# Kernel tuning notes

Hardware: AMD Instinct MI355X
Metric: run time of the kernel (lower is better)

## Reference

```python
import jax, jax.numpy as jnp
import numpy as np

EPS = 1e-4

def _mp_normalize(x):
    # EDM2-style normalize: divide by (eps + RMS-scaled L2 norm) along last dim -> unit RMS
    n = jnp.linalg.norm(x, axis=-1, keepdims=True)
    n = EPS + n * (1.0 / np.sqrt(x.shape[-1]))
    return x / n

def _mp_linear(x, w):
    # magnitude-preserving linear: row-normalized weight scaled by 1/sqrt(fan_in), no bias
    fan_in = w.shape[-1]
    w_hat = _mp_normalize(w) * (1.0 / np.sqrt(fan_in))
    return x @ w_hat.T

def setup_inputs() -> dict:
    key = jax.random.key(0)
    k1, k2, k3 = jax.random.split(key, 3)
    B, T, D = 2, 2048, 1024
    x = jax.random.normal(k1, (B, T, D), dtype=jnp.float32)
    w_qkv = jax.random.normal(k2, (3 * D, D), dtype=jnp.float32)
    w_out = jax.random.normal(k3, (D, D), dtype=jnp.float32)
    return {"x": x, "w_qkv": w_qkv, "w_out": w_out}

def reference(x, w_qkv, w_out):
    B, T, D = x.shape
    H = 16
    hd = D // H
    scale = 1.0 / np.sqrt(hd)

    qkv = _mp_linear(x, w_qkv)                      # (B, T, 3D)
    q, k, v = jnp.split(qkv, 3, axis=-1)            # each (B, T, D)

    def to_heads(t):
        return t.reshape(B, T, H, hd).transpose(0, 2, 1, 3)  # (B, H, T, hd)

    q, k, v = to_heads(q), to_heads(k), to_heads(v)
    q = _mp_normalize(q)
    k = _mp_normalize(k)

    scores = jnp.einsum("bhqd,bhkd->bhqk", q, k) * scale
    attn = jax.nn.softmax(scores, axis=-1)
    out = jnp.einsum("bhqk,bhkd->bhqd", attn, v)    # (B, H, T, hd)
    out = out.transpose(0, 2, 1, 3).reshape(B, T, D)
    return _mp_linear(out, w_out)
```

## Files before the change

kernel.cpp:

```cpp
#include <hip/hip_runtime.h>

#define BATCH  2
#define SEQ    2048
#define DMODEL 1024
#define NHEAD  16
#define HDIM   64
#define NROWS  (BATCH * SEQ)
#define QKVC   (3 * DMODEL)

typedef float f32x4 __attribute__((ext_vector_type(4)));
typedef float f32x16 __attribute__((ext_vector_type(16)));
typedef short s16x8 __attribute__((ext_vector_type(8)));
typedef short s16x4 __attribute__((ext_vector_type(4)));
typedef unsigned int u32x4 __attribute__((ext_vector_type(4)));

__device__ __forceinline__ unsigned short f2bf(float f) {
  unsigned int u = __float_as_uint(f);
  u = (u + 0x7FFFu + ((u >> 16) & 1u)) >> 16;
  return (unsigned short)u;
}
__device__ __forceinline__ float bf2f(unsigned short s) {
  return __uint_as_float(((unsigned int)s) << 16);
}
__device__ __forceinline__ unsigned pkbf(float a, float b) {
  unsigned r;
  asm("v_cvt_pk_bf16_f32 %0, %1, %2" : "=v"(r) : "v"(a), "v"(b));
  return r;
}
__device__ __forceinline__ void swp(unsigned &a, unsigned &b) {
  asm volatile("v_permlane32_swap_b32 %0, %1" : "+v"(a), "+v"(b));
}

__global__ __launch_bounds__(256) void k_prep(const float* __restrict__ Wq_src,
                                              const float* __restrict__ Wo_src,
                                              const float* __restrict__ X,
                                              unsigned short* __restrict__ Wq,
                                              unsigned short* __restrict__ Wo,
                                              unsigned short* __restrict__ Xb) {
  const int row = blockIdx.x, tid = threadIdx.x;
  if (row < QKVC + DMODEL) {
    const float* src = (row < QKVC) ? (Wq_src + (size_t)row * DMODEL)
                                    : (Wo_src + (size_t)(row - QKVC) * DMODEL);
    unsigned short* dst = (row < QKVC) ? (Wq + (size_t)row * DMODEL)
                                       : (Wo + (size_t)(row - QKVC) * DMODEL);
    float4 v = ((const float4*)src)[tid];
    float ss = v.x * v.x + v.y * v.y + v.z * v.z + v.w * v.w;
#pragma unroll
    for (int m = 1; m < 64; m <<= 1) ss += __shfl_xor(ss, m);
    __shared__ float part[4];
    if ((tid & 63) == 0) part[tid >> 6] = ss;
    __syncthreads();
    const float tot = part[0] + part[1] + part[2] + part[3];
    const float scale = 0.03125f / (1e-4f + sqrtf(tot) * 0.03125f);
    unsigned short* op = dst + tid * 4;
    op[0] = f2bf(v.x * scale); op[1] = f2bf(v.y * scale);
    op[2] = f2bf(v.z * scale); op[3] = f2bf(v.w * scale);
  } else {
    const int r = row - (QKVC + DMODEL);
    const float4 v = ((const float4*)(X + (size_t)r * DMODEL))[tid];
    ushort4 o = { f2bf(v.x), f2bf(v.y), f2bf(v.z), f2bf(v.w) };
    ((ushort4*)(Xb + (size_t)r * DMODEL))[tid] = o;
  }
}

#define LDP 88
__global__ __launch_bounds__(256, 3) void k_gemm_qkv(const unsigned short* __restrict__ A,
                                                     const unsigned short* __restrict__ Bm,
                                                     unsigned short* __restrict__ C,
                                                     unsigned short* __restrict__ Vt) {
  const int M = NROWS, N = QKVC, K = DMODEL;
  __shared__ unsigned short As[128 * LDP];
  __shared__ unsigned short Bs[128 * LDP];
  const int tid = threadIdx.x;
  const int nbn = N >> 7;
  const int bm = (blockIdx.x / nbn) << 7;
  const int bn = (blockIdx.x % nbn) << 7;
  const int wave = tid >> 6, lane = tid & 63;
  const int wr = (wave >> 1) << 6, wc = (wave & 1) << 6;
  const int l16 = lane & 15, lg = lane >> 4;

  f32x4 acc[4][4];
#pragma unroll
  for (int m = 0; m < 4; ++m)
#pragma unroll
    for (int n = 0; n < 4; ++n) acc[m][n] = (f32x4){0.f, 0.f, 0.f, 0.f};

  s16x8 ra[4], rb[4];
#pragma unroll
  for (int it = 0; it < 4; ++it) {
    const int c = it * 256 + tid;
    const int r = c >> 3, col = (c & 7) << 3;
    ra[it] = *(const s16x8*)(A + (size_t)(bm + r) * K + col);
    rb[it] = *(const s16x8*)(Bm + (size_t)(bn + r) * K + col);
  }

  for (int k0 = 0; k0 < K; k0 += 64) {
    __syncthreads();
#pragma unroll
    for (int it = 0; it < 4; ++it) {
      const int c = it * 256 + tid;
      const int r = c >> 3, col = (c & 7) << 3;
      *(s16x8*)(As + r * LDP + col) = ra[it];
      *(s16x8*)(Bs + r * LDP + col) = rb[it];
    }
    __syncthreads();
    if (k0 + 64 < K) {
#pragma unroll
      for (int it = 0; it < 4; ++it) {
        const int c = it * 256 + tid;
        const int r = c >> 3, col = (c & 7) << 3;
        ra[it] = *(const s16x8*)(A + (size_t)(bm + r) * K + k0 + 64 + col);
        rb[it] = *(const s16x8*)(Bm + (size_t)(bn + r) * K + k0 + 64 + col);
      }
    }
#pragma unroll
    for (int ks = 0; ks < 2; ++ks) {
      s16x8 af[4], bq[4];
#pragma unroll
      for (int m = 0; m < 4; ++m)
        af[m] = *(const s16x8*)(As + (wr + m * 16 + l16) * LDP + ks * 32 + lg * 8);
#pragma unroll
      for (int n = 0; n < 4; ++n)
        bq[n] = *(const s16x8*)(Bs + (wc + n * 16 + l16) * LDP + ks * 32 + lg * 8);
#pragma unroll
      for (int m = 0; m < 4; ++m)
#pragma unroll
        for (int n = 0; n < 4; ++n)
          acc[m][n] = __builtin_amdgcn_mfma_f32_16x16x32_bf16(af[m], bq[n], acc[m][n], 0, 0, 0);
    }
  }

  const int colbase = bn + wc;
  if (colbase < 2 * DMODEL) {
    const float qmul = (colbase < DMODEL) ? 0.125f : 1.0f;
#pragma unroll
    for (int m = 0; m < 4; ++m)
#pragma unroll
      for (int r = 0; r < 4; ++r) {
        float ss = 0.f;
#pragma unroll
        for (int n = 0; n < 4; ++n) ss += acc[m][n][r] * acc[m][n][r];
        ss += __shfl_xor(ss, 1); ss += __shfl_xor(ss, 2);
        ss += __shfl_xor(ss, 4); ss += __shfl_xor(ss, 8);
        const float scale = qmul / (1e-4f + sqrtf(ss) * 0.125f);
#pragma unroll
        for (int n = 0; n < 4; ++n)
          C[(size_t)(bm + wr + m * 16 + lg * 4 + r) * N + (colbase + n * 16 + l16)] =
              f2bf(acc[m][n][r] * scale);
      }
  } else {
    const int hv = (colbase - 2 * DMODEL) >> 6;
    const int token0 = bm + wr;
    const int b_ = token0 >> 11;
    const int bh = b_ * NHEAD + hv;
    const int t0 = (token0 & (SEQ - 1)) + lg * 4;
#pragma unroll
    for (int m = 0; m < 4; ++m)
#pragma unroll
      for (int n = 0; n < 4; ++n) {
        const int d = n * 16 + l16;
        s16x4 ov = { (short)f2bf(acc[m][n][0]), (short)f2bf(acc[m][n][1]),
                     (short)f2bf(acc[m][n][2]), (short)f2bf(acc[m][n][3]) };
        *(s16x4*)(Vt + (size_t)(bh * HDIM + d) * SEQ + t0 + m * 16) = ov;
      }
  }
}

__global__ __launch_bounds__(256, 3) void k_gemm_out(const unsigned short* __restrict__ A,
                                                     const unsigned short* __restrict__ Bm,
                                                     float* __restrict__ C,
                                                     int M, int N, int K) {
  __shared__ unsigned short As[128 * LDP];
  __shared__ unsigned short Bs[128 * LDP];
  const int tid = threadIdx.x;
  const int nbn = N >> 7;
  const int bm = (blockIdx.x / nbn) << 7;
  const int bn = (blockIdx.x % nbn) << 7;
  const int wave = tid >> 6, lane = tid & 63;
  const int wr = (wave >> 1) << 6, wc = (wave & 1) << 6;
  const int l16 = lane & 15, lg = lane >> 4;

  f32x4 acc[4][4];
#pragma unroll
  for (int m = 0; m < 4; ++m)
#pragma unroll
    for (int n = 0; n < 4; ++n) acc[m][n] = (f32x4){0.f, 0.f, 0.f, 0.f};

  s16x8 ra[4], rb[4];
#pragma unroll
  for (int it = 0; it < 4; ++it) {
    const int c = it * 256 + tid;
    const int r = c >> 3, col = (c & 7) << 3;
    ra[it] = *(const s16x8*)(A + (size_t)(bm + r) * K + col);
    rb[it] = *(const s16x8*)(Bm + (size_t)(bn + r) * K + col);
  }

  for (int k0 = 0; k0 < K; k0 += 64) {
    __syncthreads();
#pragma unroll
    for (int it = 0; it < 4; ++it) {
      const int c = it * 256 + tid;
      const int r = c >> 3, col = (c & 7) << 3;
      *(s16x8*)(As + r * LDP + col) = ra[it];
      *(s16x8*)(Bs + r * LDP + col) = rb[it];
    }
    __syncthreads();
    if (k0 + 64 < K) {
#pragma unroll
      for (int it = 0; it < 4; ++it) {
        const int c = it * 256 + tid;
        const int r = c >> 3, col = (c & 7) << 3;
        ra[it] = *(const s16x8*)(A + (size_t)(bm + r) * K + k0 + 64 + col);
        rb[it] = *(const s16x8*)(Bm + (size_t)(bn + r) * K + k0 + 64 + col);
      }
    }
#pragma unroll
    for (int ks = 0; ks < 2; ++ks) {
      s16x8 af[4], bq[4];
#pragma unroll
      for (int m = 0; m < 4; ++m)
        af[m] = *(const s16x8*)(As + (wr + m * 16 + l16) * LDP + ks * 32 + lg * 8);
#pragma unroll
      for (int n = 0; n < 4; ++n)
        bq[n] = *(const s16x8*)(Bs + (wc + n * 16 + l16) * LDP + ks * 32 + lg * 8);
#pragma unroll
      for (int m = 0; m < 4; ++m)
#pragma unroll
        for (int n = 0; n < 4; ++n)
          acc[m][n] = __builtin_amdgcn_mfma_f32_16x16x32_bf16(af[m], bq[n], acc[m][n], 0, 0, 0);
    }
  }
#pragma unroll
  for (int m = 0; m < 4; ++m)
#pragma unroll
    for (int n = 0; n < 4; ++n)
#pragma unroll
      for (int r = 0; r < 4; ++r)
        C[(size_t)(bm + wr + m * 16 + lg * 4 + r) * N + (bn + wc + n * 16 + l16)] =
            acc[m][n][r];
}

__global__ __launch_bounds__(512) void k_attn(const unsigned short* __restrict__ qkv,
                                              const unsigned short* __restrict__ Vt,
                                              unsigned short* __restrict__ O) {
  const int bid = blockIdx.x;
  const int logical = ((bid & 7) << 6) + (bid >> 3);
  const int bh = logical >> 4, qt = logical & 15;
  const int b = bh >> 4, h = bh & 15;
  const int tid = threadIdx.x;
  const int wave = tid >> 6, lane = tid & 63;
  const int l31 = lane & 31, hi = lane >> 5;
  const int qw = wave & 3, half = wave >> 2;
  const int q0 = qt * 128 + qw * 32;

  __shared__ s16x8 smem[2048];
  __shared__ float LL[4][64];

  s16x8* ksh = smem + half * 512;
  s16x8* vsh = smem + 1024 + half * 512;

  const unsigned short* qp =
      qkv + (size_t)(b * SEQ + q0 + l31) * QKVC + h * HDIM + hi * 8;
  const s16x8 qf0 = *(const s16x8*)(qp);
  const s16x8 qf1 = *(const s16x8*)(qp + 16);
  const s16x8 qf2 = *(const s16x8*)(qp + 32);
  const s16x8 qf3 = *(const s16x8*)(qp + 48);

  const int t8 = tid & 255;
  const int srow = t8 >> 3, chunk = t8 & 7;
  const unsigned short* ksrc =
      qkv + (size_t)(b * SEQ + half * 1024 + srow) * QKVC + DMODEL + h * HDIM + chunk * 8;
  const unsigned short* vsrc =
      Vt + (size_t)(bh * HDIM + srow) * SEQ + half * 1024 + chunk * 8;
  const int wsl = srow * 8 + (chunk ^ (srow & 7));
  const int wsh = wsl + 256;

  f32x16 acc0 = {0,0,0,0,0,0,0,0,0,0,0,0,0,0,0,0};
  f32x16 acc1 = {0,0,0,0,0,0,0,0,0,0,0,0,0,0,0,0};
  float l = 0.f;

  for (int kt = 0; kt < 1024; kt += 64) {
    const s16x8 rk0 = *(const s16x8*)(ksrc + (size_t)kt * QKVC);
    const s16x8 rk1 = *(const s16x8*)(ksrc + (size_t)(kt + 32) * QKVC);
    const s16x8 rv0 = *(const s16x8*)(vsrc + kt);
    const s16x8 rv1 = *(const s16x8*)(vsrc + (size_t)32 * SEQ + kt);
    __syncthreads();
    ksh[wsl] = rk0; ksh[wsh] = rk1;
    vsh[wsl] = rv0; vsh[wsh] = rv1;
    __syncthreads();
#pragma unroll
    for (int kh = 0; kh < 2; ++kh) {
      const int key = kh * 32 + l31;
      const int kb = key * 8, kx = key & 7;
      f32x16 st = {0,0,0,0,0,0,0,0,0,0,0,0,0,0,0,0};
      st = __builtin_amdgcn_mfma_f32_32x32x16_bf16(ksh[kb + ((0 + hi) ^ kx)], qf0, st, 0, 0, 0);
      st = __builtin_amdgcn_mfma_f32_32x32x16_bf16(ksh[kb + ((2 + hi) ^ kx)], qf1, st, 0, 0, 0);
      st = __builtin_amdgcn_mfma_f32_32x32x16_bf16(ksh[kb + ((4 + hi) ^ kx)], qf2, st, 0, 0, 0);
      st = __builtin_amdgcn_mfma_f32_32x32x16_bf16(ksh[kb + ((6 + hi) ^ kx)], qf3, st, 0, 0, 0);

#pragma unroll
      for (int r = 0; r < 16; ++r) st[r] = __expf(st[r] - 8.f);

      float s0 = (st[0] + st[1]) + (st[2] + st[3]);
      float s1 = (st[4] + st[5]) + (st[6] + st[7]);
      float s2 = (st[8] + st[9]) + (st[10] + st[11]);
      float s3 = (st[12] + st[13]) + (st[14] + st[15]);
      l += (s0 + s1) + (s2 + s3);

      unsigned P0 = pkbf(st[0], st[1]),   P1 = pkbf(st[2], st[3]);
      unsigned P2 = pkbf(st[4], st[5]),   P3 = pkbf(st[6], st[7]);
      unsigned P4 = pkbf(st[8], st[9]),   P5 = pkbf(st[10], st[11]);
      unsigned P6 = pkbf(st[12], st[13]), P7 = pkbf(st[14], st[15]);
      swp(P0, P2);
      swp(P1, P3);
      swp(P4, P6);
      swp(P5, P7);
      u32x4 w0; w0[0] = P0; w0[1] = P1; w0[2] = P2; w0[3] = P3;
      u32x4 w1; w1[0] = P4; w1[1] = P5; w1[2] = P6; w1[3] = P7;
      const s16x8 pf0 = __builtin_bit_cast(s16x8, w0);
      const s16x8 pf1 = __builtin_bit_cast(s16x8, w1);

      const int vb0 = l31 * 8,        vx0 = l31 & 7;
      const int vb1 = (l31 + 32) * 8, vx1 = vx0;
      acc0 = __builtin_amdgcn_mfma_f32_32x32x16_bf16(vsh[vb0 + ((kh * 4 + 0 + hi) ^ vx0)], pf0, acc0, 0, 0, 0);
      acc0 = __builtin_amdgcn_mfma_f32_32x32x16_bf16(vsh[vb0 + ((kh * 4 + 2 + hi) ^ vx0)], pf1, acc0, 0, 0, 0);
      acc1 = __builtin_amdgcn_mfma_f32_32x32x16_bf16(vsh[vb1 + ((kh * 4 + 0 + hi) ^ vx1)], pf0, acc1, 0, 0, 0);
      acc1 = __builtin_amdgcn_mfma_f32_32x32x16_bf16(vsh[vb1 + ((kh * 4 + 2 + hi) ^ vx1)], pf1, acc1, 0, 0, 0);
    }
  }

  l += __shfl_xor(l, 32);

  __syncthreads();
  float* OO = (float*)smem;
  if (half) {
    float* o_ = OO + qw * 2048;
#pragma unroll
    for (int r = 0; r < 16; ++r) {
      o_[r * 64 + lane] = acc0[r];
      o_[(16 + r) * 64 + lane] = acc1[r];
    }
    LL[qw][lane] = l;
  }
  __syncthreads();
  if (!half) {
    const float inv = 1.f / (l + LL[qw][lane]);
    const float* o_ = OO + qw * 2048;
    unsigned short* ob = O + (size_t)(b * SEQ + q0 + l31) * DMODEL + h * HDIM;
#pragma unroll
    for (int g = 0; g < 4; ++g) {
      float e00 = (acc0[4 * g]     + o_[(4 * g) * 64 + lane])     * inv;
      float e01 = (acc0[4 * g + 1] + o_[(4 * g + 1) * 64 + lane]) * inv;
      float e02 = (acc0[4 * g + 2] + o_[(4 * g + 2) * 64 + lane]) * inv;
      float e03 = (acc0[4 * g + 3] + o_[(4 * g + 3) * 64 + lane]) * inv;
      float e10 = (acc1[4 * g]     + o_[(16 + 4 * g) * 64 + lane])     * inv;
      float e11 = (acc1[4 * g + 1] + o_[(16 + 4 * g + 1) * 64 + lane]) * inv;
      float e12 = (acc1[4 * g + 2] + o_[(16 + 4 * g + 2) * 64 + lane]) * inv;
      float e13 = (acc1[4 * g + 3] + o_[(16 + 4 * g + 3) * 64 + lane]) * inv;
      s16x4 o0 = { (short)f2bf(e00), (short)f2bf(e01), (short)f2bf(e02), (short)f2bf(e03) };
      s16x4 o1 = { (short)f2bf(e10), (short)f2bf(e11), (short)f2bf(e12), (short)f2bf(e13) };
      *(s16x4*)(ob + g * 8 + hi * 4) = o0;
      *(s16x4*)(ob + 32 + g * 8 + hi * 4) = o1;
    }
  }
}

extern "C" void kernel_launch(void* const* d_in, const int* in_sizes, int n_in,
                              void* d_out, int out_size, void* d_ws, size_t ws_size,
                              hipStream_t stream) {
  const float* x    = (const float*)d_in[0];
  const float* wqkv = (const float*)d_in[1];
  const float* wout = (const float*)d_in[2];
  char* ws = (char*)d_ws;
  unsigned short* Wq  = (unsigned short*)(ws);
  unsigned short* Wo  = (unsigned short*)(ws + 6291456);
  unsigned short* Xb  = (unsigned short*)(ws + 8388608);
  unsigned short* QKV = (unsigned short*)(ws + 16777216);
  unsigned short* Vt  = (unsigned short*)(ws + 41943040);
  (void)in_sizes; (void)n_in; (void)out_size; (void)ws_size;

  k_prep<<<QKVC + DMODEL + NROWS, 256, 0, stream>>>(wqkv, wout, x, Wq, Wo, Xb);
  k_gemm_qkv<<<(NROWS / 128) * (QKVC / 128), 256, 0, stream>>>(Xb, Wq, QKV, Vt);
  k_attn<<<BATCH * NHEAD * 16, 512, 0, stream>>>(QKV, Vt, Xb);
  k_gemm_out<<<(NROWS / 128) * (DMODEL / 128), 256, 0, stream>>>(
      Xb, Wo, (float*)d_out, NROWS, DMODEL, DMODEL);
}
```

Measured before the change: 113.6 us.

## Double-buffer K/V shared memory tiles in attention kernel with register prefetch

The attention kernel's K/V staging goes from a single LDS buffer with two barriers per tile to a ping-pong double buffer. Tile it+1 is written from registers while tile it is computed, and global loads for tile it+2 are issued ahead, so each iteration needs only one barrier. This aims to overlap global memory latency with MFMA work and cut synchronisation. In exchange it doubles the LDS footprint to 64KB plus LL and keeps more registers live, which may reduce occupancy.

```diff
diff --git a/kernel.cpp b/kernel.cpp
--- a/kernel.cpp
+++ b/kernel.cpp
@@ -253,11 +253,8 @@
   const int qw = wave & 3, half = wave >> 2;
   const int q0 = qt * 128 + qw * 32;
 
-  __shared__ s16x8 smem[2048];
+  __shared__ s16x8 smem[4096];
   __shared__ float LL[4][64];
-
-  s16x8* ksh = smem + half * 512;
-  s16x8* vsh = smem + 1024 + half * 512;
 
   const unsigned short* qp =
       qkv + (size_t)(b * SEQ + q0 + l31) * QKVC + h * HDIM + hi * 8;
@@ -274,20 +271,42 @@
       Vt + (size_t)(bh * HDIM + srow) * SEQ + half * 1024 + chunk * 8;
   const int wsl = srow * 8 + (chunk ^ (srow & 7));
   const int wsh = wsl + 256;
+  const int koff = half * 512;
+  const int voff = 1024 + half * 512;
 
   f32x16 acc0 = {0,0,0,0,0,0,0,0,0,0,0,0,0,0,0,0};
   f32x16 acc1 = {0,0,0,0,0,0,0,0,0,0,0,0,0,0,0,0};
   float l = 0.f;
 
-  for (int kt = 0; kt < 1024; kt += 64) {
-    const s16x8 rk0 = *(const s16x8*)(ksrc + (size_t)kt * QKVC);
-    const s16x8 rk1 = *(const s16x8*)(ksrc + (size_t)(kt + 32) * QKVC);
-    const s16x8 rv0 = *(const s16x8*)(vsrc + kt);
-    const s16x8 rv1 = *(const s16x8*)(vsrc + (size_t)32 * SEQ + kt);
-    __syncthreads();
-    ksh[wsl] = rk0; ksh[wsh] = rk1;
-    vsh[wsl] = rv0; vsh[wsh] = rv1;
-    __syncthreads();
+  s16x8 rk0 = *(const s16x8*)(ksrc);
+  s16x8 rk1 = *(const s16x8*)(ksrc + (size_t)32 * QKVC);
+  s16x8 rv0 = *(const s16x8*)(vsrc);
+  s16x8 rv1 = *(const s16x8*)(vsrc + (size_t)32 * SEQ);
+  smem[koff + wsl] = rk0; smem[koff + wsh] = rk1;
+  smem[voff + wsl] = rv0; smem[voff + wsh] = rv1;
+  rk0 = *(const s16x8*)(ksrc + (size_t)64 * QKVC);
+  rk1 = *(const s16x8*)(ksrc + (size_t)96 * QKVC);
+  rv0 = *(const s16x8*)(vsrc + 64);
+  rv1 = *(const s16x8*)(vsrc + (size_t)32 * SEQ + 64);
+  __syncthreads();
+
+  int cur = 0;
+  for (int it = 0; it < 16; ++it) {
+    const int base = cur << 11;
+    const int nbase = base ^ 2048;
+    if (it + 1 < 16) {
+      smem[nbase + koff + wsl] = rk0; smem[nbase + koff + wsh] = rk1;
+      smem[nbase + voff + wsl] = rv0; smem[nbase + voff + wsh] = rv1;
+    }
+    if (it + 2 < 16) {
+      const int kt2 = (it + 2) << 6;
+      rk0 = *(const s16x8*)(ksrc + (size_t)kt2 * QKVC);
+      rk1 = *(const s16x8*)(ksrc + (size_t)(kt2 + 32) * QKVC);
+      rv0 = *(const s16x8*)(vsrc + kt2);
+      rv1 = *(const s16x8*)(vsrc + (size_t)32 * SEQ + kt2);
+    }
+    const s16x8* ksh = smem + base + koff;
+    const s16x8* vsh = smem + base + voff;
 #pragma unroll
     for (int kh = 0; kh < 2; ++kh) {
       const int key = kh * 32 + l31;
@@ -327,11 +346,12 @@
       acc1 = __builtin_amdgcn_mfma_f32_32x32x16_bf16(vsh[vb1 + ((kh * 4 + 0 + hi) ^ vx1)], pf0, acc1, 0, 0, 0);
       acc1 = __builtin_amdgcn_mfma_f32_32x32x16_bf16(vsh[vb1 + ((kh * 4 + 2 + hi) ^ vx1)], pf1, acc1, 0, 0, 0);
     }
+    __syncthreads();
+    cur ^= 1;
   }
 
   l += __shfl_xor(l, 32);
 
-  __syncthreads();
   float* OO = (float*)smem;
   if (half) {
     float* o_ = OO + qw * 2048;
```

After: 118.2 us. +4.1%, slower.
